# Kernel optimization log

Measured on AMD Instinct MI355X. Metric: run time of the kernel, lower is better.

The kernel has to match this reference:

```python
import jax, jax.numpy as jnp
import numpy as np

B, S, H, NH = 2, 2048, 2048, 32
HD = H // NH  # 64

def _causal_mask(b, s, dtype=jnp.float32):
    neg = jnp.finfo(dtype).min
    m = jnp.where(jnp.tril(jnp.ones((s, s), dtype=bool)), 0.0, neg).astype(dtype)
    return jnp.broadcast_to(m[None, None], (b, 1, s, s))

def setup_inputs() -> dict:
    key = jax.random.key(0)
    k1, k2, k3, k4, k5 = jax.random.split(key, 5)
    scale = 1.0 / np.sqrt(H)
    return {
        "hidden_states": jax.random.normal(k1, (B, S, H), jnp.float32),
        "attention_mask": _causal_mask(B, S),
        "Wq": jax.random.normal(k2, (H, H), jnp.float32) * scale,
        "Wk": jax.random.normal(k3, (H, H), jnp.float32) * scale,
        "Wv": jax.random.normal(k4, (H, H), jnp.float32) * scale,
        "Wo": jax.random.normal(k5, (H, H), jnp.float32) * scale,
    }

def reference(hidden_states, attention_mask, Wq, Wk, Wv, Wo):
    b, s, _ = hidden_states.shape
    dt = hidden_states.dtype
    def proj(W):  # torch Linear: x @ W.T -> [b, nh, s, hd]
        return (hidden_states @ W.T).reshape(b, s, NH, HD).transpose(0, 2, 1, 3)
    q, k, v = proj(Wq), proj(Wk), proj(Wv)
    attn = jnp.einsum('bhqd,bhkd->bhqk', q, k) / np.sqrt(HD)
    attn = attn + attention_mask
    attn = jnp.maximum(attn, jnp.finfo(attn.dtype).min)
    attn = jax.nn.softmax(attn.astype(jnp.float32), axis=-1).astype(dt)
    out = jnp.einsum('bhqk,bhkd->bhqd', attn, v)
    out = out.transpose(0, 2, 1, 3).reshape(b, s, H)
    return out @ Wo.T
```

## Files before the change

### kernel.cpp

```cpp
#include <hip/hip_runtime.h>
#include <hip/hip_bf16.h>
#include <stdint.h>

#define S_LEN 2048
#define NHEAD 32
#define HDIM  64

using bf16x8 = __attribute__((ext_vector_type(8))) short;
using f32x4  = __attribute__((ext_vector_type(4))) float;
using f32x16 = __attribute__((ext_vector_type(16))) float;

__device__ __forceinline__ uint16_t f2bf(float f) {
  union { float f; uint32_t u; } c; c.f = f;
  uint32_t u = c.u;
  return (uint16_t)((u + 0x7FFFu + ((u >> 16) & 1u)) >> 16);
}

__device__ __forceinline__ void load_lds16(const void* g, void* l) {
  __builtin_amdgcn_global_load_lds(
      (const __attribute__((address_space(1))) void*)g,
      (__attribute__((address_space(3))) void*)l, 16, 0, 0);
}

__device__ __forceinline__ f32x16 mfma32(bf16x8 a, bf16x8 b, f32x16 c) {
  return __builtin_amdgcn_mfma_f32_32x32x16_bf16(a, b, c, 0, 0, 0);
}

__device__ __forceinline__ uint32_t cvtpk(float lo, float hi_) {
  uint32_t d;
  asm("v_cvt_pk_bf16_f32 %0, %1, %2" : "=v"(d) : "v"(lo), "v"(hi_));
  return d;
}
__device__ __forceinline__ void plswap(uint32_t& a, uint32_t& b) {
  asm volatile("v_permlane32_swap_b32 %0, %1" : "+v"(a), "+v"(b));
}
__device__ __forceinline__ float exp2_hw(float x) {
  float r;
  asm("v_exp_f32 %0, %1" : "=v"(r) : "v"(x));
  return r;
}

__global__ __launch_bounds__(256) void conv_batch(
    const float* __restrict__ X, const float* __restrict__ Wq,
    const float* __restrict__ Wk, const float* __restrict__ Wv,
    const float* __restrict__ Wo, uint16_t* __restrict__ Xbf,
    uint16_t* __restrict__ Wqk, uint16_t* __restrict__ Wvb,
    uint16_t* __restrict__ Wob) {
  int i = blockIdx.x * 256 + threadIdx.x;
  const float* src; uint16_t* dst; int o;
  if (i < 2097152)      { src = X;  dst = Xbf;           o = i; }
  else if (i < 3145728) { src = Wq; dst = Wqk;           o = i - 2097152; }
  else if (i < 4194304) { src = Wk; dst = Wqk + 4194304; o = i - 3145728; }
  else if (i < 5242880) { src = Wv; dst = Wvb;           o = i - 4194304; }
  else                  { src = Wo; dst = Wob;           o = i - 5242880; }
  float4 v = ((const float4*)src)[o];
  uint64_t packed = (uint64_t)f2bf(v.x) | ((uint64_t)f2bf(v.y) << 16) |
                    ((uint64_t)f2bf(v.z) << 32) | ((uint64_t)f2bf(v.w) << 48);
  ((uint64_t*)dst)[o] = packed;
}

__global__ __launch_bounds__(512, 2) void gemm_qk(
    const uint16_t* __restrict__ A, const uint16_t* __restrict__ Bw,
    uint16_t* __restrict__ Qo, uint16_t* __restrict__ Ko, float qscale) {
  extern __shared__ char smem[];
  const int t = threadIdx.x;
  const int lane = t & 63, w = t >> 6;
  const int lrow = lane & 15, lgrp = lane >> 4;
  const int wr = w >> 2, wc = w & 3;
  const int id = blockIdx.x;
  const int swz = (id & 7) * 32 + (id >> 3);
  const int bm = (swz & 15) * 256, bn = (swz >> 4) * 256;
  constexpr int NT = 2048 / 32;

  const f32x4 zero4 = {0.f, 0.f, 0.f, 0.f};
  f32x4 acc[8][4];
#pragma unroll
  for (int mi = 0; mi < 8; ++mi)
#pragma unroll
    for (int ni = 0; ni < 4; ++ni) acc[mi][ni] = zero4;

  auto stage_mat = [&](const uint16_t* __restrict__ G, int grow0,
                       char* ldsbase, int kt) {
#pragma unroll
    for (int j = 0; j < 2; ++j) {
      const int s = t + j * 512;
      const int row = s >> 2;
      const int sc = (s & 3) ^ ((row >> 1) & 3);
      load_lds16(G + (size_t)(grow0 + row) * 2048 + kt + sc * 8,
                 ldsbase + j * 8192 + w * 1024);
    }
  };
  auto lda = [&](const char* Ab, int mi) -> bf16x8 {
    const int row = wr * 128 + mi * 16 + lrow;
    return *(const bf16x8*)(Ab + row * 64 + ((lgrp ^ ((row >> 1) & 3)) << 4));
  };
  auto ldb = [&](const char* Bb, int ni) -> bf16x8 {
    const int row = wc * 64 + ni * 16 + lrow;
    return *(const bf16x8*)(Bb + row * 64 + ((lgrp ^ ((row >> 1) & 3)) << 4));
  };

  stage_mat(A, bm, smem, 0);
  stage_mat(Bw, bn, smem + 16384, 0);
  stage_mat(A, bm, smem + 32768, 32);
  stage_mat(Bw, bn, smem + 32768 + 16384, 32);

  for (int kt = 0; kt < NT; ++kt) {
    char* cur = smem + (kt % 3) * 32768;
    char* nx2 = smem + ((kt + 2) % 3) * 32768;
    if (kt < NT - 1) asm volatile("s_waitcnt vmcnt(4)" ::: "memory");
    else             asm volatile("s_waitcnt vmcnt(0)" ::: "memory");
    __builtin_amdgcn_s_barrier();

    bf16x8 aF[4], bF[4];
#pragma unroll
    for (int mi = 0; mi < 4; ++mi) aF[mi] = lda(cur, mi);
#pragma unroll
    for (int ni = 0; ni < 4; ++ni) bF[ni] = ldb(cur + 16384, ni);
    if (kt + 2 < NT) stage_mat(A, bm, nx2, (kt + 2) * 32);
    __builtin_amdgcn_s_barrier();
    asm volatile("s_waitcnt lgkmcnt(0)" ::: "memory");
    __builtin_amdgcn_sched_barrier(0);
    __builtin_amdgcn_s_setprio(1);
#pragma unroll
    for (int mi = 0; mi < 4; ++mi)
#pragma unroll
      for (int ni = 0; ni < 4; ++ni)
        acc[mi][ni] = __builtin_amdgcn_mfma_f32_16x16x32_bf16(
            aF[mi], bF[ni], acc[mi][ni], 0, 0, 0);
    __builtin_amdgcn_s_setprio(0);
    __builtin_amdgcn_s_barrier();

    bf16x8 aG[4];
#pragma unroll
    for (int mi = 0; mi < 4; ++mi) aG[mi] = lda(cur, 4 + mi);
    if (kt + 2 < NT) stage_mat(Bw, bn, nx2 + 16384, (kt + 2) * 32);
    __builtin_amdgcn_s_barrier();
    asm volatile("s_waitcnt lgkmcnt(0)" ::: "memory");
    __builtin_amdgcn_sched_barrier(0);
    __builtin_amdgcn_s_setprio(1);
#pragma unroll
    for (int mi = 0; mi < 4; ++mi)
#pragma unroll
      for (int ni = 0; ni < 4; ++ni)
        acc[4 + mi][ni] = __builtin_amdgcn_mfma_f32_16x16x32_bf16(
            aG[mi], bF[ni], acc[4 + mi][ni], 0, 0, 0);
    __builtin_amdgcn_s_setprio(0);
  }

  const bool isQ = (bn < 2048);
#pragma unroll
  for (int mi = 0; mi < 8; ++mi) {
#pragma unroll
    for (int ni = 0; ni < 4; ++ni) {
      const int n = bn + wc * 64 + ni * 16 + lrow;
      const int n2 = isQ ? n : (n - 2048);
      const int h = n2 >> 6, d = n2 & 63;
#pragma unroll
      for (int r = 0; r < 4; ++r) {
        const int m = bm + wr * 128 + mi * 16 + lgrp * 4 + r;
        const int b = m >> 11, s = m & 2047;
        const size_t off = (((size_t)(b * NHEAD + h) * S_LEN + s) * HDIM) + d;
        if (isQ) Qo[off] = f2bf(acc[mi][ni][r] * qscale);
        else     Ko[off] = f2bf(acc[mi][ni][r]);
      }
    }
  }
}

template<int MODE>
__global__ __launch_bounds__(256, 3) void gemm_nt(
    const uint16_t* __restrict__ A, const uint16_t* __restrict__ B,
    void* __restrict__ C, int M, int N, int K, float scale) {
  __shared__ __align__(16) char smem[3][16384];

  const int t = threadIdx.x;
  const int lane = t & 63, w = t >> 6;
  const int lrow = lane & 15, lgrp = lane >> 4;
  const int bm = blockIdx.y * 128, bn = blockIdx.x * 128;
  const int wm = (w >> 1) * 64, wn = (w & 1) * 64;
  const int NT = K / 32;

  const f32x4 zero4 = {0.f, 0.f, 0.f, 0.f};
  f32x4 acc[4][4];
#pragma unroll
  for (int mi = 0; mi < 4; ++mi)
#pragma unroll
    for (int ni = 0; ni < 4; ++ni) acc[mi][ni] = zero4;

  auto stage_mat = [&](const uint16_t* __restrict__ G, int grow0,
                       char* ldsbase, int kt) {
#pragma unroll
    for (int j = 0; j < 2; ++j) {
      const int s = t + j * 256;
      const int row = s >> 2;
      const int sc = (s & 3) ^ ((row >> 1) & 3);
      load_lds16(G + (size_t)(grow0 + row) * K + kt + sc * 8,
                 ldsbase + j * 4096 + w * 1024);
    }
  };
  auto ldf = [&](const char* Mb, int base, int i) -> bf16x8 {
    const int row = base + i * 16 + lrow;
    return *(const bf16x8*)(Mb + row * 64 + ((lgrp ^ ((row >> 1) & 3)) << 4));
  };

  stage_mat(A, bm, smem[0], 0);
  stage_mat(B, bn, smem[0] + 8192, 0);
  stage_mat(A, bm, smem[1], 32);
  stage_mat(B, bn, smem[1] + 8192, 32);

  for (int kt = 0; kt < NT; ++kt) {
    char* cur = smem[kt % 3];
    if (kt < NT - 1) asm volatile("s_waitcnt vmcnt(4)" ::: "memory");
    else             asm volatile("s_waitcnt vmcnt(0)" ::: "memory");
    __builtin_amdgcn_s_barrier();

    if (kt + 2 < NT) {
      char* nx2 = smem[(kt + 2) % 3];
      stage_mat(A, bm, nx2, (kt + 2) * 32);
      stage_mat(B, bn, nx2 + 8192, (kt + 2) * 32);
    }

    bf16x8 aF[4], bF[4];
#pragma unroll
    for (int mi = 0; mi < 4; ++mi) aF[mi] = ldf(cur, wm, mi);
#pragma unroll
    for (int ni = 0; ni < 4; ++ni) bF[ni] = ldf(cur + 8192, wn, ni);
#pragma unroll
    for (int mi = 0; mi < 4; ++mi)
#pragma unroll
      for (int ni = 0; ni < 4; ++ni)
        acc[mi][ni] = __builtin_amdgcn_mfma_f32_16x16x32_bf16(
            aF[mi], bF[ni], acc[mi][ni], 0, 0, 0);
  }

#pragma unroll
  for (int mi = 0; mi < 4; ++mi) {
#pragma unroll
    for (int ni = 0; ni < 4; ++ni) {
      const int n = bn + wn + ni * 16 + lrow;
#pragma unroll
      for (int r = 0; r < 4; ++r) {
        const int m = bm + wm + mi * 16 + lgrp * 4 + r;
        const float v = acc[mi][ni][r] * scale;
        if (MODE == 2) {
          ((float*)C)[(size_t)m * N + n] = v;
        } else {
          const int h = m >> 6, d = m & 63;
          const int b = n >> 11, s = n & 2047;
          ((uint16_t*)C)[(((size_t)(b * NHEAD + h) * HDIM + d) * S_LEN) + s] =
              f2bf(v);
        }
      }
    }
  }
}

__global__ __launch_bounds__(256, 3) void attn_kernel(
    const uint16_t* __restrict__ Q, const uint16_t* __restrict__ K,
    const uint16_t* __restrict__ Vt, uint16_t* __restrict__ O) {
  __shared__ __align__(16) uint16_t Ks[2][64 * 64];
  __shared__ __align__(16) uint16_t Vs[2][64 * 64];

  const int t = threadIdx.x, lane = t & 63, w = t >> 6;
  const int qcol = lane & 31, hi = lane >> 5;
  const int id = blockIdx.x;
  const int bh = (id & 7) * 8 + ((id >> 3) & 7);
  const int p = id >> 6;
  const int b = bh >> 5, h = bh & 31;

  const uint16_t* Qbh = Q + (size_t)bh * S_LEN * HDIM;
  const uint16_t* Kbh = K + (size_t)bh * S_LEN * HDIM;
  const uint16_t* Vbh = Vt + (size_t)bh * HDIM * S_LEN;

  const int srow = lane >> 3;
  const int schunk = (lane & 7) ^ srow;

  const short one_bf = (short)0x3F80;
  const bf16x8 onesf = {one_bf, one_bf, one_bf, one_bf,
                        one_bf, one_bf, one_bf, one_bf};

  auto stage = [&](int k0, int bi) {
#pragma unroll
    for (int j = 0; j < 2; ++j) {
      const int r = j * 32 + w * 8 + srow;
      load_lds16(Kbh + (size_t)(k0 + r) * HDIM + schunk * 8,
                 (char*)&Ks[bi][0] + j * 4096 + w * 1024);
      load_lds16(Vbh + (size_t)r * S_LEN + k0 + schunk * 8,
                 (char*)&Vs[bi][0] + j * 4096 + w * 1024);
    }
  };

  for (int pass = 0; pass < 2; ++pass) {
    const int jq = pass ? (15 - p) : p;
    const int qw = jq * 128 + w * 32;
    const int qg = qw + qcol;

    bf16x8 qB[4];
    {
      const uint16_t* qp = Qbh + (size_t)(qw + qcol) * HDIM + hi * 8;
#pragma unroll
      for (int j = 0; j < 4; ++j) qB[j] = *(const bf16x8*)(qp + 16 * j);
    }

    f32x16 oacc0, oacc1, oS;
#pragma unroll
    for (int r = 0; r < 16; ++r) { oacc0[r] = 0.f; oacc1[r] = 0.f; oS[r] = 0.f; }

    const int nt = 2 * jq + 2;
    for (int kt = 0; kt < nt; ++kt) {
      const int cur = kt & 1;
      const int k0 = kt * 64;
      if (kt == 0) { __syncthreads(); stage(0, 0); }
      __syncthreads();
      if (kt + 1 < nt) stage((kt + 1) * 64, cur ^ 1);

      if (k0 <= qw + 31) {
        const char* Kc = (const char*)&Ks[cur][0];
        const char* Vc = (const char*)&Vs[cur][0];

        f32x16 s0, s1;
#pragma unroll
        for (int r = 0; r < 16; ++r) { s0[r] = 0.f; s1[r] = 0.f; }
        const int rk0 = qcol, rk1 = 32 + qcol;
        const int x0 = rk0 & 7;
        __builtin_amdgcn_s_setprio(1);
#pragma unroll
        for (int j = 0; j < 4; ++j) {
          bf16x8 kf0 = *(const bf16x8*)(Kc + rk0 * 128 + (((2*j+hi) ^ x0) << 4));
          bf16x8 kf1 = *(const bf16x8*)(Kc + rk1 * 128 + (((2*j+hi) ^ x0) << 4));
          s0 = mfma32(kf0, qB[j], s0);
          s1 = mfma32(kf1, qB[j], s1);
        }
        __builtin_amdgcn_s_setprio(0);

        if (k0 + 63 > qw) {
#pragma unroll
          for (int r = 0; r < 16; ++r) {
            const int krow = (r & 3) + 8 * (r >> 2) + 4 * hi;
            s0[r] = (k0 + krow <= qg) ? exp2_hw(s0[r]) : 0.f;
            s1[r] = (k0 + 32 + krow <= qg) ? exp2_hw(s1[r]) : 0.f;
          }
        } else {
#pragma unroll
          for (int r = 0; r < 16; ++r) {
            s0[r] = exp2_hw(s0[r]);
            s1[r] = exp2_hw(s1[r]);
          }
        }

        bf16x8 paf[4];
#pragma unroll
        for (int tt = 0; tt < 4; ++tt) {
          const int o = 8 * (tt & 1);
          uint32_t a0, a1, a2, a3;
          if (tt < 2) {
            a0 = cvtpk(s0[o + 0], s0[o + 1]);
            a1 = cvtpk(s0[o + 2], s0[o + 3]);
            a2 = cvtpk(s0[o + 4], s0[o + 5]);
            a3 = cvtpk(s0[o + 6], s0[o + 7]);
          } else {
            a0 = cvtpk(s1[o + 0], s1[o + 1]);
            a1 = cvtpk(s1[o + 2], s1[o + 3]);
            a2 = cvtpk(s1[o + 4], s1[o + 5]);
            a3 = cvtpk(s1[o + 6], s1[o + 7]);
          }
          plswap(a0, a2);
          plswap(a1, a3);
          union { uint32_t u[4]; bf16x8 v; } pk;
          pk.u[0] = a0; pk.u[1] = a1; pk.u[2] = a2; pk.u[3] = a3;
          paf[tt] = pk.v;
        }

        __builtin_amdgcn_s_setprio(1);
#pragma unroll
        for (int tt = 0; tt < 4; ++tt) {
          const int c = 2 * tt + hi;
          bf16x8 v0f = *(const bf16x8*)(Vc + rk0 * 128 + ((c ^ x0) << 4));
          bf16x8 v1f = *(const bf16x8*)(Vc + rk1 * 128 + ((c ^ x0) << 4));
          oacc0 = mfma32(paf[tt], v0f, oacc0);
          oacc1 = mfma32(paf[tt], v1f, oacc1);
          oS = mfma32(paf[tt], onesf, oS);
        }
        __builtin_amdgcn_s_setprio(0);
      }
    }

#pragma unroll
    for (int r = 0; r < 16; ++r) {
      const int qrow = (r & 3) + 8 * (r >> 2) + 4 * hi;
      const float inv = 1.0f / oS[r];
      const size_t base = ((size_t)b * S_LEN + qw + qrow) * 2048 + h * 64;
      O[base + qcol] = f2bf(oacc0[r] * inv);
      O[base + 32 + qcol] = f2bf(oacc1[r] * inv);
    }
  }
}

extern "C" void kernel_launch(void* const* d_in, const int* in_sizes, int n_in,
                              void* d_out, int out_size, void* d_ws,
                              size_t ws_size, hipStream_t stream) {
  const float* X  = (const float*)d_in[0];
  const float* Wq = (const float*)d_in[2];
  const float* Wk = (const float*)d_in[3];
  const float* Wv = (const float*)d_in[4];
  const float* Wo = (const float*)d_in[5];
  float* out = (float*)d_out;

  char* ws = (char*)d_ws;
  uint16_t* Xbf = (uint16_t*)ws;
  uint16_t* Wqk = (uint16_t*)(ws + 16777216);
  uint16_t* Qb  = (uint16_t*)(ws + 33554432);
  uint16_t* Kb  = (uint16_t*)(ws + 50331648);
  uint16_t* Wsm = (uint16_t*)(ws + 67108864);
  uint16_t* Wob = (uint16_t*)(ws + 75497472);
  uint16_t* Vtb = Wqk;
  uint16_t* Ob  = Xbf;

  const float qscale = 0.125f * 1.4426950408889634f;

  hipFuncSetAttribute((const void*)gemm_qk,
                      hipFuncAttributeMaxDynamicSharedMemorySize, 98304);

  conv_batch<<<24576, 256, 0, stream>>>(X, Wq, Wk, Wv, Wo, Xbf, Wqk, Wsm, Wob);
  gemm_qk<<<256, 512, 98304, stream>>>(Xbf, Wqk, Qb, Kb, qscale);
  gemm_nt<1><<<dim3(32, 16), 256, 0, stream>>>(Wsm, Xbf, Vtb, 2048, 4096, 2048, 1.0f);
  attn_kernel<<<dim3(512), 256, 0, stream>>>(Qb, Kb, Vtb, Ob);
  gemm_nt<2><<<dim3(16, 32), 256, 0, stream>>>(Ob, Wob, out, 4096, 2048, 2048, 1.0f);
}
```

Measured before the change: 228.1 us.

## Double attention K/V tile to 128 keys and interleave two QK blocks

The attention loop now stages 128 keys per iteration (two 64-key sub-tiles) into 64KB of dynamic LDS, halving the number of barrier-synchronised iterations. Within each iteration it issues the QK MFMAs for both sub-tiles before doing softmax and PV, giving the scheduler more independent work to overlap exp/convert with matrix ops. Launch bounds drop from 3 to 2 blocks per CU to fit the doubled LDS and extra registers, which reduces occupancy.

After: 221.7 us, median of 2. -2.8%, faster.

```diff
diff --git a/kernel.cpp b/kernel.cpp
--- a/kernel.cpp
+++ b/kernel.cpp
@@ -255,12 +255,10 @@
   }
 }
 
-__global__ __launch_bounds__(256, 3) void attn_kernel(
+__global__ __launch_bounds__(256, 2) void attn_kernel(
     const uint16_t* __restrict__ Q, const uint16_t* __restrict__ K,
     const uint16_t* __restrict__ Vt, uint16_t* __restrict__ O) {
-  __shared__ __align__(16) uint16_t Ks[2][64 * 64];
-  __shared__ __align__(16) uint16_t Vs[2][64 * 64];
-
+  extern __shared__ __align__(16) char asmem[];
   const int t = threadIdx.x, lane = t & 63, w = t >> 6;
   const int qcol = lane & 31, hi = lane >> 5;
   const int id = blockIdx.x;
@@ -279,16 +277,30 @@
   const bf16x8 onesf = {one_bf, one_bf, one_bf, one_bf,
                         one_bf, one_bf, one_bf, one_bf};
 
+  auto Kbuf = [&](int bi, int sub) -> char* {
+    return asmem + (bi * 2 + sub) * 8192;
+  };
+  auto Vbuf = [&](int bi, int sub) -> char* {
+    return asmem + 32768 + (bi * 2 + sub) * 8192;
+  };
+
   auto stage = [&](int k0, int bi) {
 #pragma unroll
-    for (int j = 0; j < 2; ++j) {
-      const int r = j * 32 + w * 8 + srow;
-      load_lds16(Kbh + (size_t)(k0 + r) * HDIM + schunk * 8,
-                 (char*)&Ks[bi][0] + j * 4096 + w * 1024);
-      load_lds16(Vbh + (size_t)r * S_LEN + k0 + schunk * 8,
-                 (char*)&Vs[bi][0] + j * 4096 + w * 1024);
-    }
-  };
+    for (int sub = 0; sub < 2; ++sub) {
+      const int kb = k0 + sub * 64;
+#pragma unroll
+      for (int j = 0; j < 2; ++j) {
+        const int r = j * 32 + w * 8 + srow;
+        load_lds16(Kbh + (size_t)(kb + r) * HDIM + schunk * 8,
+                   Kbuf(bi, sub) + j * 4096 + w * 1024);
+        load_lds16(Vbh + (size_t)r * S_LEN + kb + schunk * 8,
+                   Vbuf(bi, sub) + j * 4096 + w * 1024);
+      }
+    }
+  };
+
+  const int rk0 = qcol, rk1 = 32 + qcol;
+  const int x0 = qcol & 7;
 
   for (int pass = 0; pass < 2; ++pass) {
     const int jq = pass ? (15 - p) : p;
@@ -297,7 +309,7 @@
 
     bf16x8 qB[4];
     {
-      const uint16_t* qp = Qbh + (size_t)(qw + qcol) * HDIM + hi * 8;
+      const uint16_t* qp = Qbh + (size_t)qg * HDIM + hi * 8;
 #pragma unroll
       for (int j = 0; j < 4; ++j) qB[j] = *(const bf16x8*)(qp + 16 * j);
     }
@@ -306,82 +318,92 @@
 #pragma unroll
     for (int r = 0; r < 16; ++r) { oacc0[r] = 0.f; oacc1[r] = 0.f; oS[r] = 0.f; }
 
-    const int nt = 2 * jq + 2;
+    auto qk = [&](const char* Kc, f32x16& s0, f32x16& s1) {
+#pragma unroll
+      for (int r = 0; r < 16; ++r) { s0[r] = 0.f; s1[r] = 0.f; }
+      __builtin_amdgcn_s_setprio(1);
+#pragma unroll
+      for (int j = 0; j < 4; ++j) {
+        bf16x8 kf0 = *(const bf16x8*)(Kc + rk0 * 128 + (((2*j+hi) ^ x0) << 4));
+        bf16x8 kf1 = *(const bf16x8*)(Kc + rk1 * 128 + (((2*j+hi) ^ x0) << 4));
+        s0 = mfma32(kf0, qB[j], s0);
+        s1 = mfma32(kf1, qB[j], s1);
+      }
+      __builtin_amdgcn_s_setprio(0);
+    };
+    auto smx = [&](int k0s, f32x16& s0, f32x16& s1) {
+      if (k0s + 63 > qw) {
+#pragma unroll
+        for (int r = 0; r < 16; ++r) {
+          const int krow = (r & 3) + 8 * (r >> 2) + 4 * hi;
+          s0[r] = (k0s + krow <= qg) ? exp2_hw(s0[r]) : 0.f;
+          s1[r] = (k0s + 32 + krow <= qg) ? exp2_hw(s1[r]) : 0.f;
+        }
+      } else {
+#pragma unroll
+        for (int r = 0; r < 16; ++r) {
+          s0[r] = exp2_hw(s0[r]);
+          s1[r] = exp2_hw(s1[r]);
+        }
+      }
+    };
+    auto repack = [&](const f32x16& s0, const f32x16& s1, bf16x8 (&paf)[4]) {
+#pragma unroll
+      for (int tt = 0; tt < 4; ++tt) {
+        const int o = 8 * (tt & 1);
+        uint32_t a0, a1, a2, a3;
+        if (tt < 2) {
+          a0 = cvtpk(s0[o + 0], s0[o + 1]);
+          a1 = cvtpk(s0[o + 2], s0[o + 3]);
+          a2 = cvtpk(s0[o + 4], s0[o + 5]);
+          a3 = cvtpk(s0[o + 6], s0[o + 7]);
+        } else {
+          a0 = cvtpk(s1[o + 0], s1[o + 1]);
+          a1 = cvtpk(s1[o + 2], s1[o + 3]);
+          a2 = cvtpk(s1[o + 4], s1[o + 5]);
+          a3 = cvtpk(s1[o + 6], s1[o + 7]);
+        }
+        plswap(a0, a2);
+        plswap(a1, a3);
+        union { uint32_t u[4]; bf16x8 v; } pk;
+        pk.u[0] = a0; pk.u[1] = a1; pk.u[2] = a2; pk.u[3] = a3;
+        paf[tt] = pk.v;
+      }
+    };
+    auto pv = [&](const char* Vc, const bf16x8 (&paf)[4]) {
+      __builtin_amdgcn_s_setprio(1);
+#pragma unroll
+      for (int tt = 0; tt < 4; ++tt) {
+        const int c = 2 * tt + hi;
+        bf16x8 v0f = *(const bf16x8*)(Vc + rk0 * 128 + ((c ^ x0) << 4));
+        bf16x8 v1f = *(const bf16x8*)(Vc + rk1 * 128 + ((c ^ x0) << 4));
+        oacc0 = mfma32(paf[tt], v0f, oacc0);
+        oacc1 = mfma32(paf[tt], v1f, oacc1);
+        oS = mfma32(paf[tt], onesf, oS);
+      }
+      __builtin_amdgcn_s_setprio(0);
+    };
+
+    const int nt = jq + 1;
     for (int kt = 0; kt < nt; ++kt) {
       const int cur = kt & 1;
-      const int k0 = kt * 64;
+      const int k0 = kt * 128;
       if (kt == 0) { __syncthreads(); stage(0, 0); }
       __syncthreads();
-      if (kt + 1 < nt) stage((kt + 1) * 64, cur ^ 1);
-
-      if (k0 <= qw + 31) {
-        const char* Kc = (const char*)&Ks[cur][0];
-        const char* Vc = (const char*)&Vs[cur][0];
-
-        f32x16 s0, s1;
-#pragma unroll
-        for (int r = 0; r < 16; ++r) { s0[r] = 0.f; s1[r] = 0.f; }
-        const int rk0 = qcol, rk1 = 32 + qcol;
-        const int x0 = rk0 & 7;
-        __builtin_amdgcn_s_setprio(1);
-#pragma unroll
-        for (int j = 0; j < 4; ++j) {
-          bf16x8 kf0 = *(const bf16x8*)(Kc + rk0 * 128 + (((2*j+hi) ^ x0) << 4));
-          bf16x8 kf1 = *(const bf16x8*)(Kc + rk1 * 128 + (((2*j+hi) ^ x0) << 4));
-          s0 = mfma32(kf0, qB[j], s0);
-          s1 = mfma32(kf1, qB[j], s1);
-        }
-        __builtin_amdgcn_s_setprio(0);
-
-        if (k0 + 63 > qw) {
-#pragma unroll
-          for (int r = 0; r < 16; ++r) {
-            const int krow = (r & 3) + 8 * (r >> 2) + 4 * hi;
-            s0[r] = (k0 + krow <= qg) ? exp2_hw(s0[r]) : 0.f;
-            s1[r] = (k0 + 32 + krow <= qg) ? exp2_hw(s1[r]) : 0.f;
-          }
-        } else {
-#pragma unroll
-          for (int r = 0; r < 16; ++r) {
-            s0[r] = exp2_hw(s0[r]);
-            s1[r] = exp2_hw(s1[r]);
-          }
-        }
-
-        bf16x8 paf[4];
-#pragma unroll
-        for (int tt = 0; tt < 4; ++tt) {
-          const int o = 8 * (tt & 1);
-          uint32_t a0, a1, a2, a3;
-          if (tt < 2) {
-            a0 = cvtpk(s0[o + 0], s0[o + 1]);
-            a1 = cvtpk(s0[o + 2], s0[o + 3]);
-            a2 = cvtpk(s0[o + 4], s0[o + 5]);
-            a3 = cvtpk(s0[o + 6], s0[o + 7]);
-          } else {
-            a0 = cvtpk(s1[o + 0], s1[o + 1]);
-            a1 = cvtpk(s1[o + 2], s1[o + 3]);
-            a2 = cvtpk(s1[o + 4], s1[o + 5]);
-            a3 = cvtpk(s1[o + 6], s1[o + 7]);
-          }
-          plswap(a0, a2);
-          plswap(a1, a3);
-          union { uint32_t u[4]; bf16x8 v; } pk;
-          pk.u[0] = a0; pk.u[1] = a1; pk.u[2] = a2; pk.u[3] = a3;
-          paf[tt] = pk.v;
-        }
-
-        __builtin_amdgcn_s_setprio(1);
-#pragma unroll
-        for (int tt = 0; tt < 4; ++tt) {
-          const int c = 2 * tt + hi;
-          bf16x8 v0f = *(const bf16x8*)(Vc + rk0 * 128 + ((c ^ x0) << 4));
-          bf16x8 v1f = *(const bf16x8*)(Vc + rk1 * 128 + ((c ^ x0) << 4));
-          oacc0 = mfma32(paf[tt], v0f, oacc0);
-          oacc1 = mfma32(paf[tt], v1f, oacc1);
-          oS = mfma32(paf[tt], onesf, oS);
-        }
-        __builtin_amdgcn_s_setprio(0);
+      if (kt + 1 < nt) stage((kt + 1) * 128, cur ^ 1);
+
+      const bool a1 = (k0 + 64 <= qw + 31);
+      f32x16 s0a, s1a, s0b, s1b;
+      qk(Kbuf(cur, 0), s0a, s1a);
+      if (a1) qk(Kbuf(cur, 1), s0b, s1b);
+      smx(k0, s0a, s1a);
+      bf16x8 paf[4];
+      repack(s0a, s1a, paf);
+      pv(Vbuf(cur, 0), paf);
+      if (a1) {
+        smx(k0 + 64, s0b, s1b);
+        repack(s0b, s1b, paf);
+        pv(Vbuf(cur, 1), paf);
       }
     }
 
@@ -420,10 +442,12 @@
 
   hipFuncSetAttribute((const void*)gemm_qk,
                       hipFuncAttributeMaxDynamicSharedMemorySize, 98304);
+  hipFuncSetAttribute((const void*)attn_kernel,
+                      hipFuncAttributeMaxDynamicSharedMemorySize, 65536);
 
   conv_batch<<<24576, 256, 0, stream>>>(X, Wq, Wk, Wv, Wo, Xbf, Wqk, Wsm, Wob);
   gemm_qk<<<256, 512, 98304, stream>>>(Xbf, Wqk, Qb, Kb, qscale);
   gemm_nt<1><<<dim3(32, 16), 256, 0, stream>>>(Wsm, Xbf, Vtb, 2048, 4096, 2048, 1.0f);
-  attn_kernel<<<dim3(512), 256, 0, stream>>>(Qb, Kb, Vtb, Ob);
+  attn_kernel<<<512, 256, 65536, stream>>>(Qb, Kb, Vtb, Ob);
   gemm_nt<2><<<dim3(16, 32), 256, 0, stream>>>(Ob, Wob, out, 4096, 2048, 2048, 1.0f);
 }
```
